# Kernel tuning notes

Hardware: AMD Instinct MI355X
Metric: run time of the kernel (lower is better)

## Reference

```python
import jax, jax.numpy as jnp
import numpy as np
import math

HEAD_DIM = 32
N_Q_HEADS = 32
N_KV_HEADS = 8
ROPE_BASE = 10000.0
NEG_INF = -1e9


def _rope_cos_sin(seq_len, dtype):
    inv_freq = 1.0 / (ROPE_BASE ** (jnp.arange(0, HEAD_DIM, 2, dtype=jnp.float32) / HEAD_DIM))
    pos = jnp.arange(seq_len, dtype=jnp.float32)
    freqs = pos[:, None] * inv_freq[None, :]          # [S, D/2]
    emb = jnp.concatenate([freqs, freqs], axis=-1)     # [S, D]
    return jnp.cos(emb).astype(dtype), jnp.sin(emb).astype(dtype)


def _rotate_half(x):
    x1, x2 = jnp.split(x, 2, axis=-1)
    return jnp.concatenate([-x2, x1], axis=-1)


def _apply_rope(x, cos, sin):
    # x: [B, H, S, D]; cos/sin: [S, D]
    return x * cos[None, None] + _rotate_half(x) * sin[None, None]


def setup_inputs() -> dict:
    key = jax.random.key(0)
    ks = jax.random.split(key, 5)
    B, S, D = 2, 2048, 1024
    sc = 1.0 / math.sqrt(D)
    return {
        "hidden_states": jax.random.normal(ks[0], (B, S, D), jnp.float32),
        "attention_mask": jnp.ones((B, S), jnp.int32),
        "Wq": jax.random.normal(ks[1], (1024, 1024), jnp.float32) * sc,
        "Wk": jax.random.normal(ks[2], (256, 1024), jnp.float32) * sc,
        "Wv": jax.random.normal(ks[3], (256, 1024), jnp.float32) * sc,
        "Wo": jax.random.normal(ks[4], (1024, 1024), jnp.float32) * sc,
    }


def reference(hidden_states, attention_mask, Wq, Wk, Wv, Wo):
    B, S, D = hidden_states.shape
    group = N_Q_HEADS // N_KV_HEADS

    q = (hidden_states @ Wq.T).reshape(B, S, N_Q_HEADS, HEAD_DIM).transpose(0, 2, 1, 3)
    k = (hidden_states @ Wk.T).reshape(B, S, N_KV_HEADS, HEAD_DIM).transpose(0, 2, 1, 3)
    v = (hidden_states @ Wv.T).reshape(B, S, N_KV_HEADS, HEAD_DIM).transpose(0, 2, 1, 3)

    cos, sin = _rope_cos_sin(S, q.dtype)
    q = _apply_rope(q, cos, sin)
    k = _apply_rope(k, cos, sin)

    k = jnp.repeat(k, group, axis=1)  # [B, 32, S, D]
    v = jnp.repeat(v, group, axis=1)

    scores = jnp.einsum("bhqd,bhkd->bhqk", q, k) / math.sqrt(HEAD_DIM)

    causal = jnp.tril(jnp.ones((S, S), bool))
    allowed = causal[None, None] & (attention_mask[:, None, None, :] != 0)
    scores = jnp.where(allowed, scores, NEG_INF)

    attn = jax.nn.softmax(scores, axis=-1)
    out = jnp.einsum("bhqk,bhkd->bhqd", attn, v)  # [B, 32, S, 32]
    out = out.transpose(0, 2, 1, 3).reshape(B, S, D)
    return out @ Wo.T
```

## Files before the change

kernel.cpp:

```cpp
#include <hip/hip_runtime.h>

typedef __bf16 bf16x8 __attribute__((ext_vector_type(8)));
typedef __bf16 bf16x4 __attribute__((ext_vector_type(4)));
typedef short short4v __attribute__((ext_vector_type(4)));
typedef float f32x4 __attribute__((ext_vector_type(4)));

__device__ __forceinline__ f32x4 mfma16(bf16x8 a, bf16x8 b, f32x4 c) {
  return __builtin_amdgcn_mfma_f32_16x16x32_bf16(a, b, c, 0, 0, 0);
}

__device__ __forceinline__ f32x4 mfma16k16(bf16x4 a, bf16x4 b, f32x4 c) {
#if __has_builtin(__builtin_amdgcn_mfma_f32_16x16x16bf16_1k)
  short4v as = __builtin_bit_cast(short4v, a);
  short4v bs = __builtin_bit_cast(short4v, b);
  return __builtin_amdgcn_mfma_f32_16x16x16bf16_1k(as, bs, c, 0, 0, 0);
#else
  f32x4 d;
  asm volatile("v_mfma_f32_16x16x16_bf16 %0, %1, %2, %3"
               : "=v"(d)
               : "v"(a), "v"(b), "v"(c));
  return d;
#endif
}

__device__ __forceinline__ float fast_exp2(float x) {
  return __builtin_amdgcn_exp2f(x);
}

typedef const __attribute__((address_space(1))) void gvoid_t;
typedef __attribute__((address_space(3))) void svoid_t;
__device__ __forceinline__ void lds16(const __bf16* g, __bf16* l) {
  __builtin_amdgcn_global_load_lds((gvoid_t*)g, (svoid_t*)l, 16, 0, 0);
}

__global__ __launch_bounds__(256) void prep(const float* __restrict__ hidden,
                                            const float* __restrict__ Wq,
                                            const float* __restrict__ Wk,
                                            const float* __restrict__ Wv,
                                            const float* __restrict__ Wo,
                                            __bf16* __restrict__ hb,
                                            __bf16* __restrict__ Wqkvb,
                                            __bf16* __restrict__ Wob) {
  int q = blockIdx.x * 256 + threadIdx.x;
  const float* src;
  __bf16* dst;
  if (q < 1048576) {
    src = hidden; dst = hb;
  } else if ((q -= 1048576) < 262144) {
    src = Wq; dst = Wqkvb;
  } else if ((q -= 262144) < 65536) {
    src = Wk; dst = Wqkvb + 1048576;
  } else if ((q -= 65536) < 65536) {
    src = Wv; dst = Wqkvb + 1310720;
  } else {
    q -= 65536;
    src = Wo; dst = Wob;
  }
  float4 v = *(const float4*)(src + (size_t)q * 4);
  bf16x4 o = { (__bf16)v.x, (__bf16)v.y, (__bf16)v.z, (__bf16)v.w };
  *(bf16x4*)(dst + (size_t)q * 4) = o;
}

__global__ __launch_bounds__(256) void gemm_nt(const __bf16* __restrict__ A,
                                               const __bf16* __restrict__ B,
                                               __bf16* __restrict__ Cv, int N) {
  __shared__ __bf16 As[2][128][32];
  __shared__ __bf16 Bs[2][128][32];
  const int m0 = blockIdx.x * 128, n0 = blockIdx.y * 128;
  const int tid = threadIdx.x;
  const int wave = tid >> 6, lane = tid & 63, quad = lane >> 4, l16 = lane & 15;
  const int wr = wave >> 1, wc = wave & 1;
  const int srow = 32 * wave;
  const __bf16* Ag = A + (size_t)(m0 + srow + (lane >> 2)) * 1024 + (lane & 3) * 8;
  const __bf16* Bg = B + (size_t)(n0 + srow + (lane >> 2)) * 1024 + (lane & 3) * 8;
  f32x4 acc[4][4] = {};

  auto stage = [&](int buf, int k0) {
    lds16(Ag + k0, &As[buf][srow][0]);
    lds16(Ag + 16 * 1024 + k0, &As[buf][srow + 16][0]);
    lds16(Bg + k0, &Bs[buf][srow][0]);
    lds16(Bg + 16 * 1024 + k0, &Bs[buf][srow + 16][0]);
  };
  stage(0, 0);
  __syncthreads();
  int buf = 0;
  for (int k0 = 0; k0 < 1024; k0 += 32) {
    if (k0 + 32 < 1024) stage(buf ^ 1, k0 + 32);
    bf16x8 af[4], bfr[4];
#pragma unroll
    for (int i = 0; i < 4; i++)
      af[i] = *(bf16x8*)&As[buf][64 * wr + 16 * i + l16][quad * 8];
#pragma unroll
    for (int j = 0; j < 4; j++)
      bfr[j] = *(bf16x8*)&Bs[buf][64 * wc + 16 * j + l16][quad * 8];
#pragma unroll
    for (int i = 0; i < 4; i++)
#pragma unroll
      for (int j = 0; j < 4; j++) acc[i][j] = mfma16(af[i], bfr[j], acc[i][j]);
    __syncthreads();
    buf ^= 1;
  }
#pragma unroll
  for (int i = 0; i < 4; i++)
#pragma unroll
    for (int j = 0; j < 4; j++)
#pragma unroll
      for (int r = 0; r < 4; r++) {
        int row = m0 + 64 * wr + 16 * i + quad * 4 + r;
        int col = n0 + 64 * wc + 16 * j + l16;
        Cv[(size_t)row * N + col] = (__bf16)acc[i][j][r];
      }
}

__global__ __launch_bounds__(256) void gemm_wo(const __bf16* __restrict__ Op0,
                                               const __bf16* __restrict__ Op1,
                                               const float* __restrict__ rspart,
                                               const __bf16* __restrict__ B,
                                               float* __restrict__ C) {
  __shared__ __bf16 As[2][128][32];
  __shared__ __bf16 Bs[2][128][32];
  const int m0 = blockIdx.x * 128, n0 = blockIdx.y * 128;
  const int tid = threadIdx.x;
  const int wave = tid >> 6, lane = tid & 63, quad = lane >> 4, l16 = lane & 15;
  const int wr = wave >> 1, wc = wave & 1;
  const int srow = 32 * wave;
  const int r_in = srow + (lane >> 2), c_in = (lane & 3) * 8;
  const int grow0 = m0 + r_in, grow1 = grow0 + 16;
  const int b0 = grow0 >> 11, q0 = grow0 & 2047;
  const int b1 = grow1 >> 11, q1 = grow1 & 2047;
  const __bf16* Bg = B + (size_t)(n0 + r_in) * 1024 + c_in;
  f32x4 acc[4][4] = {};

  auto loadA = [&](int k0, bf16x8& a00, bf16x8& a01, bf16x8& a10, bf16x8& a11,
                   float& i0, float& i1) {
    const int h = k0 >> 5;
    a00 = *(const bf16x8*)(Op0 + (size_t)grow0 * 1024 + k0 + c_in);
    a01 = *(const bf16x8*)(Op1 + (size_t)grow0 * 1024 + k0 + c_in);
    a10 = *(const bf16x8*)(Op0 + (size_t)grow1 * 1024 + k0 + c_in);
    a11 = *(const bf16x8*)(Op1 + (size_t)grow1 * 1024 + k0 + c_in);
    i0 = 1.0f / (rspart[((size_t)b0 * 32 + h) * 2048 + q0] +
                 rspart[((size_t)(2 + b0) * 32 + h) * 2048 + q0]);
    i1 = 1.0f / (rspart[((size_t)b1 * 32 + h) * 2048 + q1] +
                 rspart[((size_t)(2 + b1) * 32 + h) * 2048 + q1]);
  };
  auto writeA = [&](int buf, bf16x8 a00, bf16x8 a01, bf16x8 a10, bf16x8 a11,
                    float i0, float i1) {
    bf16x8 w0, w1;
#pragma unroll
    for (int e = 0; e < 8; e++) {
      w0[e] = (__bf16)(((float)a00[e] + (float)a01[e]) * i0);
      w1[e] = (__bf16)(((float)a10[e] + (float)a11[e]) * i1);
    }
    *(bf16x8*)&As[buf][r_in][c_in] = w0;
    *(bf16x8*)&As[buf][r_in + 16][c_in] = w1;
  };

  {
    bf16x8 a00, a01, a10, a11;
    float i0, i1;
    loadA(0, a00, a01, a10, a11, i0, i1);
    lds16(Bg, &Bs[0][srow][0]);
    lds16(Bg + 16 * 1024, &Bs[0][srow + 16][0]);
    writeA(0, a00, a01, a10, a11, i0, i1);
  }
  __syncthreads();
  int buf = 0;
  for (int k0 = 0; k0 < 1024; k0 += 32) {
    const bool more = (k0 + 32) < 1024;
    bf16x8 a00, a01, a10, a11;
    float i0, i1;
    if (more) {
      loadA(k0 + 32, a00, a01, a10, a11, i0, i1);
      lds16(Bg + k0 + 32, &Bs[buf ^ 1][srow][0]);
      lds16(Bg + 16 * 1024 + k0 + 32, &Bs[buf ^ 1][srow + 16][0]);
    }
    bf16x8 af[4], bfr[4];
#pragma unroll
    for (int i = 0; i < 4; i++)
      af[i] = *(bf16x8*)&As[buf][64 * wr + 16 * i + l16][quad * 8];
#pragma unroll
    for (int j = 0; j < 4; j++)
      bfr[j] = *(bf16x8*)&Bs[buf][64 * wc + 16 * j + l16][quad * 8];
#pragma unroll
    for (int i = 0; i < 4; i++)
#pragma unroll
      for (int j = 0; j < 4; j++) acc[i][j] = mfma16(af[i], bfr[j], acc[i][j]);
    if (more) writeA(buf ^ 1, a00, a01, a10, a11, i0, i1);
    __syncthreads();
    buf ^= 1;
  }
#pragma unroll
  for (int i = 0; i < 4; i++)
#pragma unroll
    for (int j = 0; j < 4; j++)
#pragma unroll
      for (int r = 0; r < 4; r++) {
        int row = m0 + 64 * wr + 16 * i + quad * 4 + r;
        int col = n0 + 64 * wc + 16 * j + l16;
        C[(size_t)row * 1024 + col] = acc[i][j][r];
      }
}

__global__ __launch_bounds__(256) void ropevt(__bf16* __restrict__ QKV,
                                              __bf16* __restrict__ VT,
                                              const int* __restrict__ amask,
                                              float* __restrict__ maskb) {
  int idx = blockIdx.x * 256 + threadIdx.x;
  if (idx < 2621440) {
    __bf16* base;
    int m, i;
    if (idx < 2097152) {
      m = idx >> 9;
      int h = (idx >> 4) & 31;
      i = idx & 15;
      base = QKV + (size_t)m * 1536 + h * 32;
    } else {
      int j = idx - 2097152;
      m = j >> 7;
      int h = (j >> 4) & 7;
      i = j & 15;
      base = QKV + (size_t)m * 1536 + 1024 + h * 32;
    }
    int s = m & 2047;
    float inv = __expf(-(float)i * 0.5756462732485114f);
    float ang = (float)s * inv;
    float sn, cs;
    __sincosf(ang, &sn, &cs);
    float x0 = (float)base[i];
    float x1 = (float)base[i + 16];
    base[i] = (__bf16)(x0 * cs - x1 * sn);
    base[i + 16] = (__bf16)(x1 * cs + x0 * sn);
  } else {
    int j = idx - 2621440;
    if (j < 4096) maskb[j] = amask[j] ? -16.0f : -1.5e9f;
    int s4 = j & 511;
    int d = (j >> 9) & 31;
    int hb_ = j >> 14;
    int s = s4 * 4;
    int b_ = hb_ >> 3, hkv_ = hb_ & 7;
    const __bf16* src = QKV + (size_t)(b_ * 2048 + s) * 1536 + 1280 + hkv_ * 32 + d;
    bf16x4 ov = { src[0], src[1536], src[3072], src[4608] };
    *(bf16x4*)&VT[((size_t)hb_ * 32 + d) * 2048 + s] = ov;
  }
}

__global__ __launch_bounds__(256, 4) void attn(const __bf16* __restrict__ QKV,
                                               const __bf16* __restrict__ VT,
                                               const float* __restrict__ maskb,
                                               __bf16* __restrict__ Opart,
                                               float* __restrict__ rspart) {
  __shared__ __bf16 Ks[2][64][40];
  __shared__ __bf16 Vs[2][32][72];
  const int tid = threadIdx.x;
  const int wave = tid >> 6, lane = tid & 63;
  const int quad = lane >> 4, l16 = lane & 15;
  const int b = blockIdx.z, h = blockIdx.y, hkv = h >> 2;
  const int xp = blockIdx.x >> 1, z = blockIdx.x & 1;
  const float SC2 = 0.25503472f;

  const int sk_key = tid >> 2, sk_ch = (tid & 3) * 8;
  const int sv_d = tid >> 3, sv_seg = (tid & 7) * 8;
  const __bf16* ksrc = QKV + (size_t)(b * 2048 + sk_key) * 1536 + 1024 + hkv * 32 + sk_ch;
  const __bf16* vsrc = VT + ((size_t)(b * 8 + hkv) * 32 + sv_d) * 2048 + sv_seg;
  const float* mrow = maskb + b * 2048;

  for (int sp = 0; sp < 2; sp++) {
    const int strip = sp ? 15 - xp : xp;
    const int t_begin = z ? (strip + 1) : 0;
    const int t_end = z ? (2 * strip + 2) : (strip + 1);
    const int qw = strip * 128 + wave * 32;
    const int q_row0 = qw + l16, q_row1 = qw + 16 + l16;
    const __bf16* qbase = QKV + (size_t)(b * 2048 + qw + l16) * 1536 + h * 32 + quad * 8;
    bf16x8 qf0 = *(const bf16x8*)qbase;
    bf16x8 qf1 = *(const bf16x8*)(qbase + 16 * 1536);

    {
      uint4 kr = *(const uint4*)(ksrc + (size_t)t_begin * 64 * 1536);
      uint4 vr = *(const uint4*)(vsrc + (size_t)t_begin * 64);
      *(uint4*)&Ks[0][sk_key][sk_ch] = kr;
      *(uint4*)&Vs[0][sv_d][sv_seg] = vr;
    }
    __syncthreads();

    f32x4 o00 = {}, o01 = {}, o10 = {}, o11 = {};
    float rs0 = 0.f, rs1 = 0.f;
    int buf = 0;

    for (int t = t_begin; t < t_end; t++) {
      const int kv0 = t << 6;
      const bool more = (t + 1 < t_end);
      uint4 kr, vr;
      if (more) {
        kr = *(const uint4*)(ksrc + (size_t)(t + 1) * 64 * 1536);
        vr = *(const uint4*)(vsrc + (size_t)(t + 1) * 64);
      }
      if (kv0 <= qw + 31) {
        bf16x8 kf[4];
#pragma unroll
        for (int kt = 0; kt < 4; kt++)
          kf[kt] = *(bf16x8*)&Ks[buf][16 * kt + l16][quad * 8];
        f32x4 s0[4], s1[4];
#pragma unroll
        for (int kt = 0; kt < 4; kt++) {
          f32x4 zz = {};
          s0[kt] = mfma16(kf[kt], qf0, zz);
          s1[kt] = mfma16(kf[kt], qf1, zz);
        }
        bf16x4 pb0[4], pb1[4];
        if (kv0 + 63 <= qw) {
#pragma unroll
          for (int kt = 0; kt < 4; kt++) {
            const int kb = kv0 + 16 * kt + 4 * quad;
            float4 mb = *(const float4*)(mrow + kb);
#pragma unroll
            for (int r = 0; r < 4; r++) {
              float e0 = fast_exp2(fmaf(s0[kt][r], SC2, (&mb.x)[r]));
              float e1 = fast_exp2(fmaf(s1[kt][r], SC2, (&mb.x)[r]));
              rs0 += e0;
              rs1 += e1;
              pb0[kt][r] = (__bf16)e0;
              pb1[kt][r] = (__bf16)e1;
            }
          }
        } else {
#pragma unroll
          for (int kt = 0; kt < 4; kt++) {
            const int kb = kv0 + 16 * kt + 4 * quad;
            float4 mb = *(const float4*)(mrow + kb);
#pragma unroll
            for (int r = 0; r < 4; r++) {
              const int key = kb + r;
              float e0 = fast_exp2(fmaf(s0[kt][r], SC2, (&mb.x)[r]));
              float e1 = fast_exp2(fmaf(s1[kt][r], SC2, (&mb.x)[r]));
              e0 = (key <= q_row0) ? e0 : 0.f;
              e1 = (key <= q_row1) ? e1 : 0.f;
              rs0 += e0;
              rs1 += e1;
              pb0[kt][r] = (__bf16)e0;
              pb1[kt][r] = (__bf16)e1;
            }
          }
        }
#pragma unroll
        for (int kt = 0; kt < 4; kt++) {
          bf16x4 v0 = *(bf16x4*)&Vs[buf][l16][16 * kt + 4 * quad];
          bf16x4 v1 = *(bf16x4*)&Vs[buf][16 + l16][16 * kt + 4 * quad];
          o00 = mfma16k16(v0, pb0[kt], o00);
          o01 = mfma16k16(v1, pb0[kt], o01);
          o10 = mfma16k16(v0, pb1[kt], o10);
          o11 = mfma16k16(v1, pb1[kt], o11);
        }
      }
      if (more) {
        *(uint4*)&Ks[buf ^ 1][sk_key][sk_ch] = kr;
        *(uint4*)&Vs[buf ^ 1][sv_d][sv_seg] = vr;
      }
      __syncthreads();
      buf ^= 1;
    }
    rs0 += __shfl_xor(rs0, 16);
    rs0 += __shfl_xor(rs0, 32);
    rs1 += __shfl_xor(rs1, 16);
    rs1 += __shfl_xor(rs1, 32);
    __bf16* Op = Opart + (size_t)z * 4096 * 1024;
    size_t row0 = (size_t)(b * 2048 + q_row0);
    size_t row1 = (size_t)(b * 2048 + q_row1);
    bf16x4 w00 = { (__bf16)o00[0], (__bf16)o00[1], (__bf16)o00[2], (__bf16)o00[3] };
    bf16x4 w01 = { (__bf16)o01[0], (__bf16)o01[1], (__bf16)o01[2], (__bf16)o01[3] };
    bf16x4 w10 = { (__bf16)o10[0], (__bf16)o10[1], (__bf16)o10[2], (__bf16)o10[3] };
    bf16x4 w11 = { (__bf16)o11[0], (__bf16)o11[1], (__bf16)o11[2], (__bf16)o11[3] };
    *(bf16x4*)&Op[row0 * 1024 + h * 32 + quad * 4] = w00;
    *(bf16x4*)&Op[row0 * 1024 + h * 32 + 16 + quad * 4] = w01;
    *(bf16x4*)&Op[row1 * 1024 + h * 32 + quad * 4] = w10;
    *(bf16x4*)&Op[row1 * 1024 + h * 32 + 16 + quad * 4] = w11;
    if (quad == 0) {
      size_t ri = ((size_t)(z * 2 + b) * 32 + h) * 2048;
      rspart[ri + q_row0] = rs0;
      rspart[ri + q_row1] = rs1;
    }
  }
}

extern "C" void kernel_launch(void* const* d_in, const int* in_sizes, int n_in,
                              void* d_out, int out_size, void* d_ws, size_t ws_size,
                              hipStream_t stream) {
  const float* hidden = (const float*)d_in[0];
  const int* amask = (const int*)d_in[1];
  const float* Wq = (const float*)d_in[2];
  const float* Wk = (const float*)d_in[3];
  const float* Wv = (const float*)d_in[4];
  const float* Wo = (const float*)d_in[5];
  float* out = (float*)d_out;

  char* p = (char*)d_ws;
  auto carve = [&](size_t elems) {
    __bf16* r = (__bf16*)p;
    p += ((elems * 2 + 255) / 256) * 256;
    return r;
  };
  __bf16* hb = carve(4096ull * 1024);
  __bf16* Wqkvb = carve(1536ull * 1024);
  __bf16* Wob = carve(1024ull * 1024);
  __bf16* QKV = carve(4096ull * 1536);
  __bf16* VT = carve(4096ull * 256);
  float* maskb = (float*)carve(8192);
  __bf16* Opart = carve(2ull * 4096 * 1024);
  float* rspart = (float*)carve(2ull * 2 * 32 * 2048 * 2);

  prep<<<6656, 256, 0, stream>>>(hidden, Wq, Wk, Wv, Wo, hb, Wqkvb, Wob);

  gemm_nt<<<dim3(32, 12), 256, 0, stream>>>(hb, Wqkvb, QKV, 1536);

  ropevt<<<11264, 256, 0, stream>>>(QKV, VT, amask, maskb);

  attn<<<dim3(16, 32, 2), 256, 0, stream>>>(QKV, VT, maskb, Opart, rspart);

  gemm_wo<<<dim3(32, 8), 256, 0, stream>>>(Opart, Opart + 4096ull * 1024,
                                           rspart, Wob, out);
}
```

Before: 195.4 us.

## Fuse RoPE and V-transpose into QKV GEMM epilogue, merge split-K partials in attention

RoPE rotation and the V transpose move into the QKV GEMM epilogue, which removes the separate ropevt kernel and its extra read and write pass over QKV. Mask conversion moves into the prep kernel. The two attention split partials are now merged by whichever attention block finishes second, using an atomic flag per strip, so the output GEMM becomes a plain bf16 GEMM with direct LDS staging. This costs a memset launch, threadfences and an extra Ob buffer. The V transpose store in the epilogue is strided and uncoalesced.

After: 632.0 us. +223.4%, slower.

```diff
diff --git a/kernel.cpp b/kernel.cpp
--- a/kernel.cpp
+++ b/kernel.cpp
@@ -38,10 +38,19 @@
                                             const float* __restrict__ Wk,
                                             const float* __restrict__ Wv,
                                             const float* __restrict__ Wo,
+                                            const int* __restrict__ amask,
                                             __bf16* __restrict__ hb,
                                             __bf16* __restrict__ Wqkvb,
-                                            __bf16* __restrict__ Wob) {
-  int q = blockIdx.x * 256 + threadIdx.x;
+                                            __bf16* __restrict__ Wob,
+                                            float* __restrict__ maskb) {
+  int idx = blockIdx.x * 256 + threadIdx.x;
+  if (idx < 1024) {
+    int4 m = *(const int4*)(amask + idx * 4);
+    float4 mb = { m.x ? -16.0f : -1.5e9f, m.y ? -16.0f : -1.5e9f,
+                  m.z ? -16.0f : -1.5e9f, m.w ? -16.0f : -1.5e9f };
+    *(float4*)(maskb + idx * 4) = mb;
+  }
+  int q = idx;
   const float* src;
   __bf16* dst;
   if (q < 1048576) {
@@ -61,9 +70,10 @@
   *(bf16x4*)(dst + (size_t)q * 4) = o;
 }
 
-__global__ __launch_bounds__(256) void gemm_nt(const __bf16* __restrict__ A,
-                                               const __bf16* __restrict__ B,
-                                               __bf16* __restrict__ Cv, int N) {
+__global__ __launch_bounds__(256) void gemm_qkv(const __bf16* __restrict__ A,
+                                                const __bf16* __restrict__ B,
+                                                __bf16* __restrict__ QKV,
+                                                __bf16* __restrict__ VT) {
   __shared__ __bf16 As[2][128][32];
   __shared__ __bf16 Bs[2][128][32];
   const int m0 = blockIdx.x * 128, n0 = blockIdx.y * 128;
@@ -100,23 +110,52 @@
     __syncthreads();
     buf ^= 1;
   }
-#pragma unroll
-  for (int i = 0; i < 4; i++)
-#pragma unroll
-    for (int j = 0; j < 4; j++)
+  const int colbase = n0 + 64 * wc;
+  if (colbase < 1280) {
+    float invf = __expf(-(float)l16 * 0.5756462732485114f);
+#pragma unroll
+    for (int i = 0; i < 4; i++)
 #pragma unroll
       for (int r = 0; r < 4; r++) {
         int row = m0 + 64 * wr + 16 * i + quad * 4 + r;
-        int col = n0 + 64 * wc + 16 * j + l16;
-        Cv[(size_t)row * N + col] = (__bf16)acc[i][j][r];
-      }
-}
-
-__global__ __launch_bounds__(256) void gemm_wo(const __bf16* __restrict__ Op0,
-                                               const __bf16* __restrict__ Op1,
-                                               const float* __restrict__ rspart,
-                                               const __bf16* __restrict__ B,
-                                               float* __restrict__ C) {
+        float ang = (float)(row & 2047) * invf;
+        float sn, cs;
+        __sincosf(ang, &sn, &cs);
+        float x0 = acc[i][0][r], x1 = acc[i][1][r];
+        acc[i][0][r] = x0 * cs - x1 * sn;
+        acc[i][1][r] = x1 * cs + x0 * sn;
+        float y0 = acc[i][2][r], y1 = acc[i][3][r];
+        acc[i][2][r] = y0 * cs - y1 * sn;
+        acc[i][3][r] = y1 * cs + y0 * sn;
+      }
+#pragma unroll
+    for (int i = 0; i < 4; i++)
+#pragma unroll
+      for (int j = 0; j < 4; j++)
+#pragma unroll
+        for (int r = 0; r < 4; r++) {
+          int row = m0 + 64 * wr + 16 * i + quad * 4 + r;
+          int col = colbase + 16 * j + l16;
+          QKV[(size_t)row * 1536 + col] = (__bf16)acc[i][j][r];
+        }
+  } else {
+#pragma unroll
+    for (int i = 0; i < 4; i++)
+#pragma unroll
+      for (int j = 0; j < 4; j++)
+#pragma unroll
+        for (int r = 0; r < 4; r++) {
+          int row = m0 + 64 * wr + 16 * i + quad * 4 + r;
+          int vc = colbase + 16 * j + l16 - 1280;
+          int b_ = row >> 11, s = row & 2047;
+          VT[((size_t)(b_ * 256 + vc)) * 2048 + s] = (__bf16)acc[i][j][r];
+        }
+  }
+}
+
+__global__ __launch_bounds__(256) void gemm_out(const __bf16* __restrict__ A,
+                                                const __bf16* __restrict__ B,
+                                                float* __restrict__ C) {
   __shared__ __bf16 As[2][128][32];
   __shared__ __bf16 Bs[2][128][32];
   const int m0 = blockIdx.x * 128, n0 = blockIdx.y * 128;
@@ -124,56 +163,21 @@
   const int wave = tid >> 6, lane = tid & 63, quad = lane >> 4, l16 = lane & 15;
   const int wr = wave >> 1, wc = wave & 1;
   const int srow = 32 * wave;
-  const int r_in = srow + (lane >> 2), c_in = (lane & 3) * 8;
-  const int grow0 = m0 + r_in, grow1 = grow0 + 16;
-  const int b0 = grow0 >> 11, q0 = grow0 & 2047;
-  const int b1 = grow1 >> 11, q1 = grow1 & 2047;
-  const __bf16* Bg = B + (size_t)(n0 + r_in) * 1024 + c_in;
+  const __bf16* Ag = A + (size_t)(m0 + srow + (lane >> 2)) * 1024 + (lane & 3) * 8;
+  const __bf16* Bg = B + (size_t)(n0 + srow + (lane >> 2)) * 1024 + (lane & 3) * 8;
   f32x4 acc[4][4] = {};
 
-  auto loadA = [&](int k0, bf16x8& a00, bf16x8& a01, bf16x8& a10, bf16x8& a11,
-                   float& i0, float& i1) {
-    const int h = k0 >> 5;
-    a00 = *(const bf16x8*)(Op0 + (size_t)grow0 * 1024 + k0 + c_in);
-    a01 = *(const bf16x8*)(Op1 + (size_t)grow0 * 1024 + k0 + c_in);
-    a10 = *(const bf16x8*)(Op0 + (size_t)grow1 * 1024 + k0 + c_in);
-    a11 = *(const bf16x8*)(Op1 + (size_t)grow1 * 1024 + k0 + c_in);
-    i0 = 1.0f / (rspart[((size_t)b0 * 32 + h) * 2048 + q0] +
-                 rspart[((size_t)(2 + b0) * 32 + h) * 2048 + q0]);
-    i1 = 1.0f / (rspart[((size_t)b1 * 32 + h) * 2048 + q1] +
-                 rspart[((size_t)(2 + b1) * 32 + h) * 2048 + q1]);
+  auto stage = [&](int buf, int k0) {
+    lds16(Ag + k0, &As[buf][srow][0]);
+    lds16(Ag + 16 * 1024 + k0, &As[buf][srow + 16][0]);
+    lds16(Bg + k0, &Bs[buf][srow][0]);
+    lds16(Bg + 16 * 1024 + k0, &Bs[buf][srow + 16][0]);
   };
-  auto writeA = [&](int buf, bf16x8 a00, bf16x8 a01, bf16x8 a10, bf16x8 a11,
-                    float i0, float i1) {
-    bf16x8 w0, w1;
-#pragma unroll
-    for (int e = 0; e < 8; e++) {
-      w0[e] = (__bf16)(((float)a00[e] + (float)a01[e]) * i0);
-      w1[e] = (__bf16)(((float)a10[e] + (float)a11[e]) * i1);
-    }
-    *(bf16x8*)&As[buf][r_in][c_in] = w0;
-    *(bf16x8*)&As[buf][r_in + 16][c_in] = w1;
-  };
-
-  {
-    bf16x8 a00, a01, a10, a11;
-    float i0, i1;
-    loadA(0, a00, a01, a10, a11, i0, i1);
-    lds16(Bg, &Bs[0][srow][0]);
-    lds16(Bg + 16 * 1024, &Bs[0][srow + 16][0]);
-    writeA(0, a00, a01, a10, a11, i0, i1);
-  }
+  stage(0, 0);
   __syncthreads();
   int buf = 0;
   for (int k0 = 0; k0 < 1024; k0 += 32) {
-    const bool more = (k0 + 32) < 1024;
-    bf16x8 a00, a01, a10, a11;
-    float i0, i1;
-    if (more) {
-      loadA(k0 + 32, a00, a01, a10, a11, i0, i1);
-      lds16(Bg + k0 + 32, &Bs[buf ^ 1][srow][0]);
-      lds16(Bg + 16 * 1024 + k0 + 32, &Bs[buf ^ 1][srow + 16][0]);
-    }
+    if (k0 + 32 < 1024) stage(buf ^ 1, k0 + 32);
     bf16x8 af[4], bfr[4];
 #pragma unroll
     for (int i = 0; i < 4; i++)
@@ -185,7 +189,6 @@
     for (int i = 0; i < 4; i++)
 #pragma unroll
       for (int j = 0; j < 4; j++) acc[i][j] = mfma16(af[i], bfr[j], acc[i][j]);
-    if (more) writeA(buf ^ 1, a00, a01, a10, a11, i0, i1);
     __syncthreads();
     buf ^= 1;
   }
@@ -201,56 +204,16 @@
       }
 }
 
-__global__ __launch_bounds__(256) void ropevt(__bf16* __restrict__ QKV,
-                                              __bf16* __restrict__ VT,
-                                              const int* __restrict__ amask,
-                                              float* __restrict__ maskb) {
-  int idx = blockIdx.x * 256 + threadIdx.x;
-  if (idx < 2621440) {
-    __bf16* base;
-    int m, i;
-    if (idx < 2097152) {
-      m = idx >> 9;
-      int h = (idx >> 4) & 31;
-      i = idx & 15;
-      base = QKV + (size_t)m * 1536 + h * 32;
-    } else {
-      int j = idx - 2097152;
-      m = j >> 7;
-      int h = (j >> 4) & 7;
-      i = j & 15;
-      base = QKV + (size_t)m * 1536 + 1024 + h * 32;
-    }
-    int s = m & 2047;
-    float inv = __expf(-(float)i * 0.5756462732485114f);
-    float ang = (float)s * inv;
-    float sn, cs;
-    __sincosf(ang, &sn, &cs);
-    float x0 = (float)base[i];
-    float x1 = (float)base[i + 16];
-    base[i] = (__bf16)(x0 * cs - x1 * sn);
-    base[i + 16] = (__bf16)(x1 * cs + x0 * sn);
-  } else {
-    int j = idx - 2621440;
-    if (j < 4096) maskb[j] = amask[j] ? -16.0f : -1.5e9f;
-    int s4 = j & 511;
-    int d = (j >> 9) & 31;
-    int hb_ = j >> 14;
-    int s = s4 * 4;
-    int b_ = hb_ >> 3, hkv_ = hb_ & 7;
-    const __bf16* src = QKV + (size_t)(b_ * 2048 + s) * 1536 + 1280 + hkv_ * 32 + d;
-    bf16x4 ov = { src[0], src[1536], src[3072], src[4608] };
-    *(bf16x4*)&VT[((size_t)hb_ * 32 + d) * 2048 + s] = ov;
-  }
-}
-
 __global__ __launch_bounds__(256, 4) void attn(const __bf16* __restrict__ QKV,
                                                const __bf16* __restrict__ VT,
                                                const float* __restrict__ maskb,
                                                __bf16* __restrict__ Opart,
-                                               float* __restrict__ rspart) {
+                                               float* __restrict__ rspart,
+                                               __bf16* __restrict__ Ob,
+                                               int* __restrict__ flags) {
   __shared__ __bf16 Ks[2][64][40];
   __shared__ __bf16 Vs[2][32][72];
+  __shared__ int flag_sh;
   const int tid = threadIdx.x;
   const int wave = tid >> 6, lane = tid & 63;
   const int quad = lane >> 4, l16 = lane & 15;
@@ -378,6 +341,32 @@
       rspart[ri + q_row0] = rs0;
       rspart[ri + q_row1] = rs1;
     }
+    __threadfence();
+    __syncthreads();
+    if (tid == 0)
+      flag_sh = atomicAdd(&flags[(b * 32 + h) * 16 + strip], 1);
+    __syncthreads();
+    if (flag_sh == 1) {
+      __threadfence();
+      const __bf16* P0 = Opart;
+      const __bf16* P1 = Opart + 4096ull * 1024;
+      const float* r0 = rspart + ((size_t)b * 32 + h) * 2048;
+      const float* r1 = rspart + ((size_t)(2 + b) * 32 + h) * 2048;
+      int rr = tid >> 2, cc = (tid & 3) * 8;
+#pragma unroll
+      for (int half = 0; half < 2; half++) {
+        int row = strip * 128 + half * 64 + rr;
+        size_t off = ((size_t)(b * 2048 + row)) * 1024 + h * 32 + cc;
+        bf16x8 a = *(const bf16x8*)&P0[off];
+        bf16x8 c = *(const bf16x8*)&P1[off];
+        float is = 1.0f / (r0[row] + r1[row]);
+        bf16x8 w;
+#pragma unroll
+        for (int e = 0; e < 8; e++)
+          w[e] = (__bf16)(((float)a[e] + (float)c[e]) * is);
+        *(bf16x8*)&Ob[off] = w;
+      }
+    }
   }
 }
 
@@ -403,18 +392,21 @@
   __bf16* Wob = carve(1024ull * 1024);
   __bf16* QKV = carve(4096ull * 1536);
   __bf16* VT = carve(4096ull * 256);
+  __bf16* Ob = carve(4096ull * 1024);
   float* maskb = (float*)carve(8192);
   __bf16* Opart = carve(2ull * 4096 * 1024);
   float* rspart = (float*)carve(2ull * 2 * 32 * 2048 * 2);
-
-  prep<<<6656, 256, 0, stream>>>(hidden, Wq, Wk, Wv, Wo, hb, Wqkvb, Wob);
-
-  gemm_nt<<<dim3(32, 12), 256, 0, stream>>>(hb, Wqkvb, QKV, 1536);
-
-  ropevt<<<11264, 256, 0, stream>>>(QKV, VT, amask, maskb);
-
-  attn<<<dim3(16, 32, 2), 256, 0, stream>>>(QKV, VT, maskb, Opart, rspart);
-
-  gemm_wo<<<dim3(32, 8), 256, 0, stream>>>(Opart, Opart + 4096ull * 1024,
-                                           rspart, Wob, out);
-}
+  int* flags = (int*)carve(2048);
+
+  hipMemsetAsync(flags, 0, 1024 * sizeof(int), stream);
+
+  prep<<<6656, 256, 0, stream>>>(hidden, Wq, Wk, Wv, Wo, amask,
+                                 hb, Wqkvb, Wob, maskb);
+
+  gemm_qkv<<<dim3(32, 12), 256, 0, stream>>>(hb, Wqkvb, QKV, VT);
+
+  attn<<<dim3(16, 32, 2), 256, 0, stream>>>(QKV, VT, maskb, Opart, rspart,
+                                            Ob, flags);
+
+  gemm_out<<<dim3(32, 8), 256, 0, stream>>>(Ob, Wob, out);
+}
```
